# Performance work log

Hardware: AMD Instinct MI355X
Metric: run time of the kernel (lower is better)

The kernel has to match this reference:

```python
import jax, jax.numpy as jnp
import numpy as np

EPSILON = 0.001
CAP = 2000.0
H, W, C, B = 224, 224, 1024, 256


def setup_inputs() -> dict:
    key = jax.random.key(0)
    k1, k2, k3, k4 = jax.random.split(key, 4)
    x = jax.random.normal(k1, (B, H, W), dtype=jnp.float32)
    positions = 0.5 + 0.3 * jax.random.normal(k2, (1, 1, C, 2), dtype=jnp.float32)
    sigmas = 0.02 * jax.random.normal(k3, (1, 1, C), dtype=jnp.float32)
    curve_weights = 0.2 * jax.random.normal(k4, (1, 1, C), dtype=jnp.float32)
    y_axis = jnp.linspace(0.0, 1.0, H + 1)[:-1]
    x_axis = jnp.linspace(0.0, 1.0, W + 1)[:-1]
    ys, xs = jnp.meshgrid(y_axis, x_axis, indexing='ij')
    return {"x": x, "positions": positions, "sigmas": sigmas,
            "curve_weights": curve_weights, "xs": xs.astype(jnp.float32),
            "ys": ys.astype(jnp.float32)}


def calc_curves(positions, sigmas, curve_weights, xs, ys):
    # sigmas/curve_weights: (1,1,C); xs/ys: (H,W)
    two_sig2 = 2.0 * sigmas ** 2 + EPSILON            # (1,1,C)
    factor = 1.0 / (2.0 * jnp.pi * sigmas ** 2 + EPSILON)
    grid = (xs[:, :, None] - positions[..., 1]) ** 2 + \
           (ys[:, :, None] - positions[..., 0]) ** 2   # (H,W,C)
    curves = factor * jnp.exp(-grid / two_sig2) * curve_weights
    return jnp.clip(curves, -CAP, CAP)                 # (H,W,C)


def reference(x, positions, sigmas, curve_weights, xs, ys):
    x = x.reshape(-1, H, W)
    curves = calc_curves(positions, sigmas, curve_weights, xs, ys)
    num_pixels = float(H * W)
    # sum over H,W of curves[None] * x[...,None]  ==  GEMM contraction
    out = jnp.einsum('bhw,hwc->bc', x, curves) / num_pixels
    return out
```

## Files before the change

kernel.cpp:

```cpp
#include <hip/hip_runtime.h>
#include <hip/hip_bf16.h>
#include <stdint.h>

#define HH 224
#define WW 224
#define CC 1024
#define BB 256
#define KK (HH*WW)
#define EPSILON_F 0.001f
#define LOG2E 1.4426950408889634f
#define INVN (1.0f/50176.0f)
#define CLAMP_V (2000.0f/50176.0f)

#define KCHUNKS 32
#define ROWS_PER_CHUNK 7
#define STEPS_PER_ROW 7

#define LDS_STRIDE 40

typedef __bf16 bf16x8 __attribute__((ext_vector_type(8)));
typedef float  f32x4  __attribute__((ext_vector_type(4)));

__global__ __launch_bounds__(256)
void blob_gemm_kernel(const float* __restrict__ x,
                      const float* __restrict__ pos,
                      const float* __restrict__ sig,
                      const float* __restrict__ cwt,
                      const float* __restrict__ xs,
                      const float* __restrict__ ys,
                      float* __restrict__ out) {
    __shared__ __bf16 As[128 * LDS_STRIDE];
    __shared__ __bf16 Bs[128 * LDS_STRIDE];
    __shared__ float  xrow[WW];
    __shared__ float  ycol[ROWS_PER_CHUNK];

    const int tid  = threadIdx.x;
    const int wave = tid >> 6;
    const int lane = tid & 63;

    const int c0 = blockIdx.x * 128;
    const int m0 = blockIdx.y * 128;
    const int k0 = blockIdx.z * (ROWS_PER_CHUNK * WW);

    if (tid < WW) xrow[tid] = xs[tid];
    if (tid >= WW && tid < WW + ROWS_PER_CHUNK) {
        int r = tid - WW;
        int h = blockIdx.z * ROWS_PER_CHUNK + r;
        ycol[r] = ys[h * WW];
    }

    const int q    = tid & 3;
    const int cr0  = tid >> 2;
    float A2[2], S2[2], P1[2], EYC[2];
    float P0[2];
#pragma unroll
    for (int g = 0; g < 2; ++g) {
        int cidx = (g << 6) + cr0;
        int c = c0 + cidx;
        float s  = sig[c];
        float w  = cwt[c];
        float s2 = s * s;
        A2[g] = w / (6.283185307179586f * s2 + EPSILON_F) * INVN;
        S2[g] = LOG2E / (2.0f * s2 + EPSILON_F);
        P0[g] = pos[2 * c];
        P1[g] = pos[2 * c + 1];
    }

    __bf16* as_w0 = As + cr0 * LDS_STRIDE + q * 8;
    __bf16* as_w1 = As + (64 + cr0) * LDS_STRIDE + q * 8;
    __bf16* bs_w0 = Bs + cr0 * LDS_STRIDE + q * 8;
    __bf16* bs_w1 = Bs + (64 + cr0) * LDS_STRIDE + q * 8;

    const float* ag0 = x + (size_t)(m0 + cr0) * KK + k0 + q * 8;
    const float* ag1 = x + (size_t)(m0 + 64 + cr0) * KK + k0 + q * 8;

    const int wm = (wave & 1) * 64;
    const int wn = (wave >> 1) * 64;
    const int fl = lane & 15;
    const int fk = (lane >> 4) * 8;
    const __bf16* ar = As + (wm + fl) * LDS_STRIDE + fk;
    const __bf16* br = Bs + (wn + fl) * LDS_STRIDE + fk;

    f32x4 acc[4][4];
#pragma unroll
    for (int i = 0; i < 4; ++i)
#pragma unroll
        for (int j = 0; j < 4; ++j) acc[i][j] = (f32x4){0.f, 0.f, 0.f, 0.f};

    __syncthreads();

#pragma unroll 1
    for (int r = 0; r < ROWS_PER_CHUNK; ++r) {
        const float ysv = ycol[r];
        {
            float dy0 = ysv - P0[0]; EYC[0] = dy0 * dy0 * S2[0];
            float dy1 = ysv - P0[1]; EYC[1] = dy1 * dy1 * S2[1];
        }
#pragma unroll 1
        for (int wb = 0; wb < STEPS_PER_ROW; ++wb) {
            const int kb = r * WW + wb * 32;

            float4 a00 = *(const float4*)(ag0 + kb);
            float4 a01 = *(const float4*)(ag0 + kb + 4);
            float4 a10 = *(const float4*)(ag1 + kb);
            float4 a11 = *(const float4*)(ag1 + kb + 4);

            float4 xv0 = *(const float4*)(xrow + wb * 32 + q * 8);
            float4 xv1 = *(const float4*)(xrow + wb * 32 + q * 8 + 4);
            float xv[8] = {xv0.x, xv0.y, xv0.z, xv0.w, xv1.x, xv1.y, xv1.z, xv1.w};

            union { __bf16 h[8]; uint4 u; } cv0, cv1;
#pragma unroll
            for (int i = 0; i < 8; ++i) {
                float dx0 = xv[i] - P1[0];
                float t0  = __builtin_fmaf(dx0 * S2[0], dx0, EYC[0]);
                float v0  = __builtin_amdgcn_exp2f(-t0) * A2[0];
                v0 = fminf(fmaxf(v0, -CLAMP_V), CLAMP_V);
                cv0.h[i] = (__bf16)v0;
                float dx1 = xv[i] - P1[1];
                float t1  = __builtin_fmaf(dx1 * S2[1], dx1, EYC[1]);
                float v1  = __builtin_amdgcn_exp2f(-t1) * A2[1];
                v1 = fminf(fmaxf(v1, -CLAMP_V), CLAMP_V);
                cv1.h[i] = (__bf16)v1;
            }

            union { __bf16 h[8]; uint4 u; } av0, av1;
            av0.h[0] = (__bf16)a00.x; av0.h[1] = (__bf16)a00.y;
            av0.h[2] = (__bf16)a00.z; av0.h[3] = (__bf16)a00.w;
            av0.h[4] = (__bf16)a01.x; av0.h[5] = (__bf16)a01.y;
            av0.h[6] = (__bf16)a01.z; av0.h[7] = (__bf16)a01.w;
            av1.h[0] = (__bf16)a10.x; av1.h[1] = (__bf16)a10.y;
            av1.h[2] = (__bf16)a10.z; av1.h[3] = (__bf16)a10.w;
            av1.h[4] = (__bf16)a11.x; av1.h[5] = (__bf16)a11.y;
            av1.h[6] = (__bf16)a11.z; av1.h[7] = (__bf16)a11.w;

            __syncthreads();
            *(uint4*)bs_w0 = cv0.u;
            *(uint4*)bs_w1 = cv1.u;
            *(uint4*)as_w0 = av0.u;
            *(uint4*)as_w1 = av1.u;
            __syncthreads();

            bf16x8 af[4], bf[4];
#pragma unroll
            for (int i = 0; i < 4; ++i) {
                af[i] = *(const bf16x8*)(ar + i * 16 * LDS_STRIDE);
                bf[i] = *(const bf16x8*)(br + i * 16 * LDS_STRIDE);
            }
#pragma unroll
            for (int mi = 0; mi < 4; ++mi)
#pragma unroll
                for (int ni = 0; ni < 4; ++ni)
                    acc[mi][ni] = __builtin_amdgcn_mfma_f32_16x16x32_bf16(
                        af[mi], bf[ni], acc[mi][ni], 0, 0, 0);
        }
    }

    const int orow = (lane >> 4) * 4;
#pragma unroll
    for (int mi = 0; mi < 4; ++mi) {
        int m = m0 + wm + mi * 16 + orow;
#pragma unroll
        for (int ni = 0; ni < 4; ++ni) {
            int c = c0 + wn + ni * 16 + fl;
#pragma unroll
            for (int v = 0; v < 4; ++v)
                atomicAdd(out + (size_t)(m + v) * CC + c, acc[mi][ni][v]);
        }
    }
}

extern "C" void kernel_launch(void* const* d_in, const int* in_sizes, int n_in,
                              void* d_out, int out_size, void* d_ws, size_t ws_size,
                              hipStream_t stream) {
    const float* x   = (const float*)d_in[0];
    const float* pos = (const float*)d_in[1];
    const float* sg  = (const float*)d_in[2];
    const float* cw  = (const float*)d_in[3];
    const float* xs  = (const float*)d_in[4];
    const float* ys  = (const float*)d_in[5];
    float* out = (float*)d_out;

    hipMemsetAsync(out, 0, (size_t)BB * CC * sizeof(float), stream);

    dim3 grid(CC / 128, BB / 128, KCHUNKS);
    blob_gemm_kernel<<<grid, 256, 0, stream>>>(x, pos, sg, cw, xs, ys, out);
}
```

Baseline: 161.1 us.

## Pre-convert x to bf16 in workspace and split K finer

```diff
diff --git a/kernel.cpp b/kernel.cpp
--- a/kernel.cpp
+++ b/kernel.cpp
@@ -12,17 +12,32 @@
 #define INVN (1.0f/50176.0f)
 #define CLAMP_V (2000.0f/50176.0f)
 
-#define KCHUNKS 32
-#define ROWS_PER_CHUNK 7
+#define KCHUNKS 112
+#define ROWS_PER_CHUNK 2
 #define STEPS_PER_ROW 7
 
-#define LDS_STRIDE 40
+#define LDS_STRIDE 36
 
 typedef __bf16 bf16x8 __attribute__((ext_vector_type(8)));
 typedef float  f32x4  __attribute__((ext_vector_type(4)));
 
 __global__ __launch_bounds__(256)
-void blob_gemm_kernel(const float* __restrict__ x,
+void cvt_bf16_kernel(const float* __restrict__ x, __hip_bfloat16* __restrict__ xb, int n8) {
+    int i = blockIdx.x * 256 + threadIdx.x;
+    if (i >= n8) return;
+    const float4* p = (const float4*)(x + (size_t)i * 8);
+    float4 a = p[0], b = p[1];
+    union { __hip_bfloat16 h[8]; uint4 u; } o;
+    o.h[0] = (__hip_bfloat16)a.x; o.h[1] = (__hip_bfloat16)a.y;
+    o.h[2] = (__hip_bfloat16)a.z; o.h[3] = (__hip_bfloat16)a.w;
+    o.h[4] = (__hip_bfloat16)b.x; o.h[5] = (__hip_bfloat16)b.y;
+    o.h[6] = (__hip_bfloat16)b.z; o.h[7] = (__hip_bfloat16)b.w;
+    *(uint4*)(xb + (size_t)i * 8) = o.u;
+}
+
+template <bool BF16A>
+__global__ __launch_bounds__(256, BF16A ? 7 : 4)
+void blob_gemm_kernel(const void* __restrict__ xin,
                       const float* __restrict__ pos,
                       const float* __restrict__ sig,
                       const float* __restrict__ cwt,
@@ -51,12 +66,10 @@
 
     const int q    = tid & 3;
     const int cr0  = tid >> 2;
-    float A2[2], S2[2], P1[2], EYC[2];
-    float P0[2];
+    float A2[2], S2[2], P1[2], P0[2], EYC[2];
 #pragma unroll
     for (int g = 0; g < 2; ++g) {
-        int cidx = (g << 6) + cr0;
-        int c = c0 + cidx;
+        int c = c0 + (g << 6) + cr0;
         float s  = sig[c];
         float w  = cwt[c];
         float s2 = s * s;
@@ -71,8 +84,10 @@
     __bf16* bs_w0 = Bs + cr0 * LDS_STRIDE + q * 8;
     __bf16* bs_w1 = Bs + (64 + cr0) * LDS_STRIDE + q * 8;
 
-    const float* ag0 = x + (size_t)(m0 + cr0) * KK + k0 + q * 8;
-    const float* ag1 = x + (size_t)(m0 + 64 + cr0) * KK + k0 + q * 8;
+    const float* agf0 = (const float*)xin + (size_t)(m0 + cr0) * KK + k0 + q * 8;
+    const float* agf1 = (const float*)xin + (size_t)(m0 + 64 + cr0) * KK + k0 + q * 8;
+    const __hip_bfloat16* agb0 = (const __hip_bfloat16*)xin + (size_t)(m0 + cr0) * KK + k0 + q * 8;
+    const __hip_bfloat16* agb1 = (const __hip_bfloat16*)xin + (size_t)(m0 + 64 + cr0) * KK + k0 + q * 8;
 
     const int wm = (wave & 1) * 64;
     const int wn = (wave >> 1) * 64;
@@ -100,10 +115,24 @@
         for (int wb = 0; wb < STEPS_PER_ROW; ++wb) {
             const int kb = r * WW + wb * 32;
 
-            float4 a00 = *(const float4*)(ag0 + kb);
-            float4 a01 = *(const float4*)(ag0 + kb + 4);
-            float4 a10 = *(const float4*)(ag1 + kb);
-            float4 a11 = *(const float4*)(ag1 + kb + 4);
+            union { __bf16 h[8]; uint4 u; } av0, av1;
+            if (BF16A) {
+                av0.u = *(const uint4*)(agb0 + kb);
+                av1.u = *(const uint4*)(agb1 + kb);
+            } else {
+                float4 a00 = *(const float4*)(agf0 + kb);
+                float4 a01 = *(const float4*)(agf0 + kb + 4);
+                float4 a10 = *(const float4*)(agf1 + kb);
+                float4 a11 = *(const float4*)(agf1 + kb + 4);
+                av0.h[0] = (__bf16)a00.x; av0.h[1] = (__bf16)a00.y;
+                av0.h[2] = (__bf16)a00.z; av0.h[3] = (__bf16)a00.w;
+                av0.h[4] = (__bf16)a01.x; av0.h[5] = (__bf16)a01.y;
+                av0.h[6] = (__bf16)a01.z; av0.h[7] = (__bf16)a01.w;
+                av1.h[0] = (__bf16)a10.x; av1.h[1] = (__bf16)a10.y;
+                av1.h[2] = (__bf16)a10.z; av1.h[3] = (__bf16)a10.w;
+                av1.h[4] = (__bf16)a11.x; av1.h[5] = (__bf16)a11.y;
+                av1.h[6] = (__bf16)a11.z; av1.h[7] = (__bf16)a11.w;
+            }
 
             float4 xv0 = *(const float4*)(xrow + wb * 32 + q * 8);
             float4 xv1 = *(const float4*)(xrow + wb * 32 + q * 8 + 4);
@@ -124,16 +153,6 @@
                 cv1.h[i] = (__bf16)v1;
             }
 
-            union { __bf16 h[8]; uint4 u; } av0, av1;
-            av0.h[0] = (__bf16)a00.x; av0.h[1] = (__bf16)a00.y;
-            av0.h[2] = (__bf16)a00.z; av0.h[3] = (__bf16)a00.w;
-            av0.h[4] = (__bf16)a01.x; av0.h[5] = (__bf16)a01.y;
-            av0.h[6] = (__bf16)a01.z; av0.h[7] = (__bf16)a01.w;
-            av1.h[0] = (__bf16)a10.x; av1.h[1] = (__bf16)a10.y;
-            av1.h[2] = (__bf16)a10.z; av1.h[3] = (__bf16)a10.w;
-            av1.h[4] = (__bf16)a11.x; av1.h[5] = (__bf16)a11.y;
-            av1.h[6] = (__bf16)a11.z; av1.h[7] = (__bf16)a11.w;
-
             __syncthreads();
             *(uint4*)bs_w0 = cv0.u;
             *(uint4*)bs_w1 = cv1.u;
@@ -184,5 +203,15 @@
     hipMemsetAsync(out, 0, (size_t)BB * CC * sizeof(float), stream);
 
     dim3 grid(CC / 128, BB / 128, KCHUNKS);
-    blob_gemm_kernel<<<grid, 256, 0, stream>>>(x, pos, sg, cw, xs, ys, out);
+
+    const size_t nx = (size_t)BB * KK;
+    const size_t need = nx * sizeof(__hip_bfloat16);
+    if (ws_size >= need) {
+        __hip_bfloat16* xb = (__hip_bfloat16*)d_ws;
+        int n8 = (int)(nx / 8);
+        cvt_bf16_kernel<<<(n8 + 255) / 256, 256, 0, stream>>>(x, xb, n8);
+        blob_gemm_kernel<true><<<grid, 256, 0, stream>>>(xb, pos, sg, cw, xs, ys, out);
+    } else {
+        blob_gemm_kernel<false><<<grid, 256, 0, stream>>>(x, pos, sg, cw, xs, ys, out);
+    }
 }
```

After: 426.3 us. 2.65x slower.
